# Optimization experiments

Hardware: AMD Instinct MI355X
Metric: run time of the kernel (lower is better)

## Reference

```python
import jax, jax.numpy as jnp
import numpy as np

B, H, S, D, T = 2, 32, 8192, 128, 512


def setup_inputs() -> dict:
    key = jax.random.key(0)
    k1, k2, k3, k4 = jax.random.split(key, 4)
    return {
        "cache_k": jax.random.normal(k1, (B, H, S, D), dtype=jnp.float32),
        "cache_v": jax.random.normal(k2, (B, H, S, D), dtype=jnp.float32),
        "new_k": jax.random.normal(k3, (B, H, T, D), dtype=jnp.float32),
        "new_v": jax.random.normal(k4, (B, H, T, D), dtype=jnp.float32),
        "position_ids": jnp.arange(T, dtype=jnp.int64),  # contiguous prefill positions
    }


def reference(cache_k, cache_v, new_k, new_v, position_ids):
    # torch: cache.scatter(2, pos.expand(B,H,T,D), new) with unique positions
    # == write new_k/new_v rows into the cache along the sequence axis.
    updated_k = cache_k.at[:, :, position_ids, :].set(new_k)
    updated_v = cache_v.at[:, :, position_ids, :].set(new_v)
    return (updated_k, updated_v)
```

## Files before the change

### kernel.cpp

```cpp
#include <hip/hip_runtime.h>


#define S_LEN 8192
#define T_LEN 512
#define D_DIM 128
#define BH    64
#define ELEMS_PER_TENSOR (BH * S_LEN * D_DIM)
#define VECS_PER_TENSOR  (ELEMS_PER_TENSOR / 4)

__global__ void ssc_init_map(int* __restrict__ map) {
    int s = blockIdx.x * blockDim.x + threadIdx.x;
    if (s < S_LEN) map[s] = -1;
}

__global__ void ssc_build_map(const void* __restrict__ pos, int* __restrict__ map) {
    int t = blockIdx.x * blockDim.x + threadIdx.x;
    if (t >= T_LEN) return;
    const long long* p64 = (const long long*)pos;
    const int*       p32 = (const int*)pos;
    long long a = p64[0], b = p64[1];
    bool is64 = (a >= 0) && (a < S_LEN) && (b >= 0) && (b < S_LEN) && (a != b);
    int s = is64 ? (int)p64[t] : p32[t];
    if (s >= 0 && s < S_LEN) map[s] = t;
}

__global__ __launch_bounds__(256) void ssc_scatter_copy(
    const float4* __restrict__ ck, const float4* __restrict__ cv,
    const float4* __restrict__ nk, const float4* __restrict__ nv,
    const int*    __restrict__ map,
    float4* __restrict__ ok, float4* __restrict__ ov) {
    const int stride = gridDim.x * blockDim.x;
    for (int idx = blockIdx.x * blockDim.x + threadIdx.x;
         idx < VECS_PER_TENSOR; idx += stride) {
        const int d4 = idx & 31;
        const int s  = (idx >> 5) & (S_LEN - 1);
        const int bh = idx >> 18;
        const int t  = map[s];
        float4 kv, vv;
        if (t >= 0) {
            const int src = (bh * T_LEN + t) * (D_DIM / 4) + d4;
            kv = nk[src];
            vv = nv[src];
        } else {
            kv = ck[idx];
            vv = cv[idx];
        }
        ok[idx] = kv;
        ov[idx] = vv;
    }
}

extern "C" void kernel_launch(void* const* d_in, const int* in_sizes, int n_in,
                              void* d_out, int out_size, void* d_ws, size_t ws_size,
                              hipStream_t stream) {
    const float4* ck = (const float4*)d_in[0];
    const float4* cv = (const float4*)d_in[1];
    const float4* nk = (const float4*)d_in[2];
    const float4* nv = (const float4*)d_in[3];
    const void*   pos = d_in[4];

    float* out = (float*)d_out;
    float4* ok = (float4*)out;
    float4* ov = (float4*)(out + ELEMS_PER_TENSOR);

    int* map = (int*)d_ws;

    ssc_init_map<<<(S_LEN + 255) / 256, 256, 0, stream>>>(map);
    ssc_build_map<<<(T_LEN + 255) / 256, 256, 0, stream>>>(pos, map);
    ssc_scatter_copy<<<2048, 256, 0, stream>>>(ck, cv, nk, nv, map, ok, ov);
}
```

Baseline: 234.8 us.

## Fuse map init/build and restructure scatter copy with per-s branch and nontemporal I/O

Merges the map init and build kernels into one single-block launch, which removes one kernel launch. The copy kernel now assigns each thread a fixed (s, d4) position and loops over 32 bh slices. The map lookup and branch therefore happen once per thread instead of once per element. All loads and stores become nontemporal to avoid polluting the cache on this pure streaming copy, and each thread has several independent memory operations in flight. This gives up the grid-stride loop for a fixed 1024x2 grid, and the single-block map build runs serially before the copy.

```diff
diff --git a/kernel.cpp b/kernel.cpp
--- a/kernel.cpp
+++ b/kernel.cpp
@@ -6,66 +6,75 @@
 #define D_DIM 128
 #define BH    64
 #define ELEMS_PER_TENSOR (BH * S_LEN * D_DIM)
-#define VECS_PER_TENSOR  (ELEMS_PER_TENSOR / 4)
+#define VECS_PER_BH      (S_LEN * (D_DIM / 4))
+#define NEW_VECS_PER_BH  (T_LEN * (D_DIM / 4))
 
-__global__ void ssc_init_map(int* __restrict__ map) {
-    int s = blockIdx.x * blockDim.x + threadIdx.x;
-    if (s < S_LEN) map[s] = -1;
-}
+typedef float f4_t __attribute__((ext_vector_type(4)));
 
 __global__ void ssc_build_map(const void* __restrict__ pos, int* __restrict__ map) {
-    int t = blockIdx.x * blockDim.x + threadIdx.x;
-    if (t >= T_LEN) return;
-    const long long* p64 = (const long long*)pos;
-    const int*       p32 = (const int*)pos;
-    long long a = p64[0], b = p64[1];
-    bool is64 = (a >= 0) && (a < S_LEN) && (b >= 0) && (b < S_LEN) && (a != b);
-    int s = is64 ? (int)p64[t] : p32[t];
-    if (s >= 0 && s < S_LEN) map[s] = t;
+    const int tid = threadIdx.x;
+    for (int s = tid; s < S_LEN; s += 1024) map[s] = -1;
+    __syncthreads();
+    if (tid < T_LEN) {
+        const long long* p64 = (const long long*)pos;
+        const int*       p32 = (const int*)pos;
+        long long a = p64[0], b = p64[1];
+        bool is64 = (a >= 0) && (a < S_LEN) && (b >= 0) && (b < S_LEN) && (a != b);
+        int s = is64 ? (int)p64[tid] : p32[tid];
+        if (s >= 0 && s < S_LEN) map[s] = tid;
+    }
 }
 
 __global__ __launch_bounds__(256) void ssc_scatter_copy(
-    const float4* __restrict__ ck, const float4* __restrict__ cv,
-    const float4* __restrict__ nk, const float4* __restrict__ nv,
-    const int*    __restrict__ map,
-    float4* __restrict__ ok, float4* __restrict__ ov) {
-    const int stride = gridDim.x * blockDim.x;
-    for (int idx = blockIdx.x * blockDim.x + threadIdx.x;
-         idx < VECS_PER_TENSOR; idx += stride) {
-        const int d4 = idx & 31;
-        const int s  = (idx >> 5) & (S_LEN - 1);
-        const int bh = idx >> 18;
-        const int t  = map[s];
-        float4 kv, vv;
-        if (t >= 0) {
-            const int src = (bh * T_LEN + t) * (D_DIM / 4) + d4;
-            kv = nk[src];
-            vv = nv[src];
-        } else {
-            kv = ck[idx];
-            vv = cv[idx];
+    const f4_t* __restrict__ ck, const f4_t* __restrict__ cv,
+    const f4_t* __restrict__ nk, const f4_t* __restrict__ nv,
+    const int*  __restrict__ map,
+    f4_t* __restrict__ ok, f4_t* __restrict__ ov) {
+    const int tid = blockIdx.x * 256 + threadIdx.x;
+    const int d4  = tid & 31;
+    const int s   = tid >> 5;
+    const int t   = map[s];
+
+    const int bh0    = blockIdx.y * (BH / 2);
+    const int dstOff = s * 32 + d4;
+
+    if (t >= 0) {
+        const int srcOff = t * 32 + d4;
+        #pragma unroll 8
+        for (int i = 0; i < BH / 2; ++i) {
+            const int bh = bh0 + i;
+            f4_t kv = __builtin_nontemporal_load(nk + srcOff + bh * NEW_VECS_PER_BH);
+            f4_t vv = __builtin_nontemporal_load(nv + srcOff + bh * NEW_VECS_PER_BH);
+            __builtin_nontemporal_store(kv, ok + dstOff + bh * VECS_PER_BH);
+            __builtin_nontemporal_store(vv, ov + dstOff + bh * VECS_PER_BH);
         }
-        ok[idx] = kv;
-        ov[idx] = vv;
+    } else {
+        #pragma unroll 8
+        for (int i = 0; i < BH / 2; ++i) {
+            const int bh = bh0 + i;
+            f4_t kv = __builtin_nontemporal_load(ck + dstOff + bh * VECS_PER_BH);
+            f4_t vv = __builtin_nontemporal_load(cv + dstOff + bh * VECS_PER_BH);
+            __builtin_nontemporal_store(kv, ok + dstOff + bh * VECS_PER_BH);
+            __builtin_nontemporal_store(vv, ov + dstOff + bh * VECS_PER_BH);
+        }
     }
 }
 
 extern "C" void kernel_launch(void* const* d_in, const int* in_sizes, int n_in,
                               void* d_out, int out_size, void* d_ws, size_t ws_size,
                               hipStream_t stream) {
-    const float4* ck = (const float4*)d_in[0];
-    const float4* cv = (const float4*)d_in[1];
-    const float4* nk = (const float4*)d_in[2];
-    const float4* nv = (const float4*)d_in[3];
-    const void*   pos = d_in[4];
+    const f4_t* ck = (const f4_t*)d_in[0];
+    const f4_t* cv = (const f4_t*)d_in[1];
+    const f4_t* nk = (const f4_t*)d_in[2];
+    const f4_t* nv = (const f4_t*)d_in[3];
+    const void* pos = d_in[4];
 
     float* out = (float*)d_out;
-    float4* ok = (float4*)out;
-    float4* ov = (float4*)(out + ELEMS_PER_TENSOR);
+    f4_t* ok = (f4_t*)out;
+    f4_t* ov = (f4_t*)(out + ELEMS_PER_TENSOR);
 
     int* map = (int*)d_ws;
 
-    ssc_init_map<<<(S_LEN + 255) / 256, 256, 0, stream>>>(map);
-    ssc_build_map<<<(T_LEN + 255) / 256, 256, 0, stream>>>(pos, map);
-    ssc_scatter_copy<<<2048, 256, 0, stream>>>(ck, cv, nk, nv, map, ok, ov);
+    ssc_build_map<<<1, 1024, 0, stream>>>(pos, map);
+    ssc_scatter_copy<<<dim3(1024, 2), 256, 0, stream>>>(ck, cv, nk, nv, map, ok, ov);
 }
```

Measured after the change: 227.6 us. 3.1% less time.
